# Kernel optimization log

Hardware: AMD Instinct MI355X
Metric: run time of the kernel (lower is better)

## Reference

```python
import math
import jax, jax.numpy as jnp
import numpy as np

B, T, C, H, TOP_K = 2, 2048, 1024, 16, 256
D = C // H  # head_dim = 64


def setup_inputs() -> dict:
    key = jax.random.key(0)
    kx, kq, kk, kv, ko = jax.random.split(key, 5)
    s = 1.0 / math.sqrt(C)
    return {
        "x": jax.random.normal(kx, (B, T, C), dtype=jnp.float32),
        "Wq": jax.random.normal(kq, (C, C), dtype=jnp.float32) * s,
        "Wk": jax.random.normal(kk, (C, C), dtype=jnp.float32) * s,
        "Wv": jax.random.normal(kv, (C, C), dtype=jnp.float32) * s,
        "Wo": jax.random.normal(ko, (C, C), dtype=jnp.float32) * s,
    }


def _sparsify_last_dim_topk(x, keep_k):
    # keep the keep_k largest-|.| entries along the last dim, zero the rest
    a = jnp.abs(x)
    kth = jax.lax.top_k(a, keep_k)[0][..., -1:]  # k-th largest magnitude
    return jnp.where(a >= kth, x, jnp.zeros_like(x))


def reference(x, Wq, Wk, Wv, Wo):
    b, t, c = x.shape
    k_keep = min(TOP_K, t)

    def proj(W):  # nn.Linear (no bias): x @ W.T, then split heads -> [B,H,T,D]
        return (x @ W.T).reshape(b, t, H, D).transpose(0, 2, 1, 3)

    q, k, v = proj(Wq), proj(Wk), proj(Wv)

    # feature-dim sparsification: keep ratio = k_keep / T of head_dim features
    feat_keep = max(1, math.ceil(D * k_keep / t))
    q = _sparsify_last_dim_topk(q, feat_keep)
    k = _sparsify_last_dim_topk(k, feat_keep)
    v = _sparsify_last_dim_topk(v, feat_keep)

    scores = jnp.einsum("bhtd,bhsd->bhts", q, k) / math.sqrt(D)  # [B,H,T,T]
    causal = jnp.tril(jnp.ones((t, t), dtype=bool))  # True = visible
    neg_inf = jnp.float32(-jnp.inf)
    scores = jnp.where(causal, scores, neg_inf)

    # row-wise top-k: keep k_keep largest scores per query row, -inf elsewhere
    kth = jax.lax.top_k(scores, k_keep)[0][..., -1:]
    sparse_scores = jnp.where(scores >= kth, scores, neg_inf)

    attn = jax.nn.softmax(sparse_scores, axis=-1)  # dropout p=0 (eval)
    out = jnp.einsum("bhts,bhsd->bhtd", attn, v)
    out = out.transpose(0, 2, 1, 3).reshape(b, t, c)
    return out @ Wo.T
```

## Files before the change

kernel.cpp:

```cpp
#include <hip/hip_runtime.h>
#include <cstdint>

constexpr int Tn = 2048;
constexpr int Cn = 1024;
constexpr int Mn = 4096;
constexpr int KKEEP = 256;
constexpr int FKEEP = 8;
constexpr unsigned U_NEG_INF = 0x007FFFFFu;

constexpr int NW     = 4;
constexpr int NJMAX  = 32;

__device__ __forceinline__ unsigned umap(float f) {
    unsigned b = __float_as_uint(f);
    return (b & 0x80000000u) ? ~b : (b | 0x80000000u);
}
__device__ __forceinline__ float uunmap(unsigned u) {
    return __uint_as_float((u & 0x80000000u) ? (u ^ 0x80000000u) : ~u);
}

__device__ __forceinline__ unsigned short f2bf(float f) {
    unsigned u = __float_as_uint(f);
    u += 0x7FFFu + ((u >> 16) & 1u);
    return (unsigned short)(u >> 16);
}
struct bfpair { unsigned short h, l; };
__device__ __forceinline__ bfpair split_bf16(float x) {
    bfpair r;
    r.h = f2bf(x);
    r.l = f2bf(x - __uint_as_float((unsigned)r.h << 16));
    return r;
}

__device__ __forceinline__ int   rli(int v, int l)   { return __builtin_amdgcn_readlane(v, l); }
__device__ __forceinline__ float rlf(float v, int l) {
    return __int_as_float(__builtin_amdgcn_readlane(__float_as_int(v), l));
}

typedef __attribute__((ext_vector_type(8))) short          short8v;
typedef __attribute__((ext_vector_type(8))) unsigned short ushort8v;
typedef __attribute__((ext_vector_type(4))) float          f32x4;

__global__ __launch_bounds__(256, 2)
void gemm_nt_3bf16(const float* __restrict__ A,
                   const float* __restrict__ W0, const float* __restrict__ W1,
                   const float* __restrict__ W2,
                   float* __restrict__ O0, float* __restrict__ O1,
                   float* __restrict__ O2)
{
    const float* Wm = (blockIdx.z == 0) ? W0 : (blockIdx.z == 1 ? W1 : W2);
    float*       O  = (blockIdx.z == 0) ? O0 : (blockIdx.z == 1 ? O1 : O2);

    __shared__ unsigned short Ah[128][40], Al[128][40];
    __shared__ unsigned short Bh[128][40], Bl[128][40];

    const int tid  = threadIdx.x;
    const int lane = tid & 63;
    const int wv   = tid >> 6;
    const int wm   = wv >> 1, wn = wv & 1;
    const int fm   = lane & 15;
    const int fq   = lane >> 4;
    const int m0   = blockIdx.y * 128;
    const int n0   = blockIdx.x * 128;

    f32x4 acc[4][4] = {};

    for (int k0 = 0; k0 < Cn; k0 += 32) {
        __syncthreads();
#pragma unroll
        for (int r = 0; r < 2; ++r) {
            const int idx = tid + r * 256;
            const int row = idx >> 2, c8 = (idx & 3) * 8;
            {
                const float* s = &A[(size_t)(m0 + row) * Cn + k0 + c8];
                const float4 x0 = *(const float4*)s, x1 = *(const float4*)(s + 4);
                ushort8v h, l;
                bfpair p;
                p = split_bf16(x0.x); h[0] = p.h; l[0] = p.l;
                p = split_bf16(x0.y); h[1] = p.h; l[1] = p.l;
                p = split_bf16(x0.z); h[2] = p.h; l[2] = p.l;
                p = split_bf16(x0.w); h[3] = p.h; l[3] = p.l;
                p = split_bf16(x1.x); h[4] = p.h; l[4] = p.l;
                p = split_bf16(x1.y); h[5] = p.h; l[5] = p.l;
                p = split_bf16(x1.z); h[6] = p.h; l[6] = p.l;
                p = split_bf16(x1.w); h[7] = p.h; l[7] = p.l;
                *(ushort8v*)&Ah[row][c8] = h;
                *(ushort8v*)&Al[row][c8] = l;
            }
            {
                const float* s = &Wm[(size_t)(n0 + row) * Cn + k0 + c8];
                const float4 x0 = *(const float4*)s, x1 = *(const float4*)(s + 4);
                ushort8v h, l;
                bfpair p;
                p = split_bf16(x0.x); h[0] = p.h; l[0] = p.l;
                p = split_bf16(x0.y); h[1] = p.h; l[1] = p.l;
                p = split_bf16(x0.z); h[2] = p.h; l[2] = p.l;
                p = split_bf16(x0.w); h[3] = p.h; l[3] = p.l;
                p = split_bf16(x1.x); h[4] = p.h; l[4] = p.l;
                p = split_bf16(x1.y); h[5] = p.h; l[5] = p.l;
                p = split_bf16(x1.z); h[6] = p.h; l[6] = p.l;
                p = split_bf16(x1.w); h[7] = p.h; l[7] = p.l;
                *(ushort8v*)&Bh[row][c8] = h;
                *(ushort8v*)&Bl[row][c8] = l;
            }
        }
        __syncthreads();

        short8v ah[4], al[4], bh[4], bl[4];
#pragma unroll
        for (int ti = 0; ti < 4; ++ti) {
            ah[ti] = *(const short8v*)&Ah[wm * 64 + ti * 16 + fm][fq * 8];
            al[ti] = *(const short8v*)&Al[wm * 64 + ti * 16 + fm][fq * 8];
            bh[ti] = *(const short8v*)&Bh[wn * 64 + ti * 16 + fm][fq * 8];
            bl[ti] = *(const short8v*)&Bl[wn * 64 + ti * 16 + fm][fq * 8];
        }
#pragma unroll
        for (int ti = 0; ti < 4; ++ti)
#pragma unroll
            for (int tj = 0; tj < 4; ++tj) {
                acc[ti][tj] = __builtin_amdgcn_mfma_f32_16x16x32_bf16(
                    ah[ti], bh[tj], acc[ti][tj], 0, 0, 0);
                acc[ti][tj] = __builtin_amdgcn_mfma_f32_16x16x32_bf16(
                    ah[ti], bl[tj], acc[ti][tj], 0, 0, 0);
                acc[ti][tj] = __builtin_amdgcn_mfma_f32_16x16x32_bf16(
                    al[ti], bh[tj], acc[ti][tj], 0, 0, 0);
            }
    }

#pragma unroll
    for (int ti = 0; ti < 4; ++ti)
#pragma unroll
        for (int tj = 0; tj < 4; ++tj)
#pragma unroll
            for (int r = 0; r < 4; ++r) {
                const int row = m0 + wm * 64 + ti * 16 + fq * 4 + r;
                const int col = n0 + wn * 64 + tj * 16 + fm;
                O[(size_t)row * Cn + col] = acc[ti][tj][r];
            }
}

__global__ __launch_bounds__(256)
void sparsify_topk(float* __restrict__ Q, float* __restrict__ V)
{
    const int wid  = (blockIdx.x * 256 + threadIdx.x) >> 6;
    const int lane = threadIdx.x & 63;
    const int tensor = wid >> 16;
    const int vec    = wid & 65535;
    float* base = tensor ? V : Q;

    const size_t off = (size_t)vec * 64 + lane;
    const float v = base[off];
    const float a = fabsf(v);

    int cnt = 0;
#pragma unroll
    for (int j = 0; j < 64; ++j) {
        const float aj = __shfl(a, j);
        cnt += (aj > a) ? 1 : 0;
    }
    float cand = (cnt < FKEEP) ? a : 3.402823466e38f;
#pragma unroll
    for (int o = 32; o; o >>= 1) cand = fminf(cand, __shfl_xor(cand, o));
    base[off] = (a >= cand) ? v : 0.0f;
}

__global__ __launch_bounds__(256)
void sparsify_k_t(const float* __restrict__ K, float* __restrict__ KT)
{
    __shared__ float tile[64][65];

    const int tid = threadIdx.x;
    const int w = tid >> 6, lane = tid & 63;
    const int tt = blockIdx.x;
    const int bh = blockIdx.y;
    const int b = bh >> 4, h = bh & 15;
    const int t0 = tt * 64;

#pragma unroll
    for (int k = 0; k < 4; ++k) {
        const int c = tid + k * 256;
        const int row = c >> 4, off = (c & 15) * 4;
        const float4 v4 = *(const float4*)
            &K[(size_t)((b * Tn + t0 + row) * 16 + h) * 64 + off];
        tile[row][off + 0] = v4.x; tile[row][off + 1] = v4.y;
        tile[row][off + 2] = v4.z; tile[row][off + 3] = v4.w;
    }
    __syncthreads();

#pragma unroll 1
    for (int r = w; r < 64; r += 4) {
        const float v = tile[r][lane];
        const float a = fabsf(v);
        int cnt = 0;
#pragma unroll
        for (int j = 0; j < 64; ++j) {
            const float aj = __shfl(a, j);
            cnt += (aj > a) ? 1 : 0;
        }
        float cand = (cnt < FKEEP) ? a : 3.402823466e38f;
#pragma unroll
        for (int o = 32; o; o >>= 1) cand = fminf(cand, __shfl_xor(cand, o));
        tile[r][lane] = (a >= cand) ? v : 0.0f;
    }
    __syncthreads();

#pragma unroll
    for (int k = 0; k < 16; ++k) {
        const int d = w + k * 4;
        KT[(((size_t)bh * 64 + d) << 11) + t0 + lane] = tile[lane][d];
    }
}

__global__ __launch_bounds__(256, 4)
void attn_kernel(const float* __restrict__ Qm, const float* __restrict__ KTm,
                 const float* __restrict__ Vm, float* __restrict__ AO)
{
    __shared__ unsigned hist[NW * 256];
    __shared__ unsigned ctab[NW * 256];
    __shared__ unsigned ptab[NW * 256];

    const int tid  = threadIdx.x;
    const int w    = tid >> 6;
    const int lane = tid & 63;
    const int bh   = blockIdx.y;
    const int b    = bh >> 4;
    const int h    = bh & 15;
    const int t    = blockIdx.x * NW + w;
    const size_t rowoff = ((size_t)(b * Tn + t) << 10) + (h << 6);
    const size_t kvoff  = ((size_t)(b * Tn) << 10) + (h << 6);

    const float q0  = Qm[rowoff + lane];
    const float qsc = q0 * 0.125f;
    const unsigned long long nzm = __ballot(q0 != 0.0f);
    const int nnz = __popcll(nzm);

    const int nj = (t >> 6) + 1;
    const float* ktb = KTm + ((size_t)bh << 17);

    const bool dosel = (t >= KKEEP);
    unsigned* hrow = hist + w * 256;
    hrow[lane] = 0; hrow[64 + lane] = 0; hrow[128 + lane] = 0; hrow[192 + lane] = 0;
    __asm__ volatile("s_waitcnt lgkmcnt(0)" ::: "memory");

    unsigned sv[NJMAX];
    unsigned rowmax = 0u;
    if (nnz == 8) {
        float mq[8]; int moff[8];
        {
            unsigned long long mm = nzm;
#pragma unroll
            for (int i = 0; i < 8; ++i) {
                const int m = (int)__builtin_ctzll(mm); mm &= mm - 1;
                mq[i] = rlf(qsc, m);
                moff[i] = m << 11;
            }
        }
#pragma unroll
        for (int jq = 0; jq < NJMAX / 4; ++jq) {
            const int j0 = jq * 4;
            if (j0 >= nj) {
                sv[j0] = U_NEG_INF; sv[j0 + 1] = U_NEG_INF;
                sv[j0 + 2] = U_NEG_INF; sv[j0 + 3] = U_NEG_INF;
                continue;
            }
            const int c0 = (j0 << 6) + lane;
            if (j0 + 4 <= nj) {
                float s0 = 0.0f, s1 = 0.0f, s2 = 0.0f, s3 = 0.0f;
#pragma unroll
                for (int i = 0; i < 8; ++i) {
                    const float* kpi = ktb + moff[i];
                    s0 += mq[i] * kpi[c0];
                    s1 += mq[i] * kpi[c0 + 64];
                    s2 += mq[i] * kpi[c0 + 128];
                    s3 += mq[i] * kpi[c0 + 192];
                }
                const unsigned v0 = (c0       <= t) ? umap(s0) : U_NEG_INF;
                const unsigned v1 = (c0 +  64 <= t) ? umap(s1) : U_NEG_INF;
                const unsigned v2 = (c0 + 128 <= t) ? umap(s2) : U_NEG_INF;
                const unsigned v3 = (c0 + 192 <= t) ? umap(s3) : U_NEG_INF;
                sv[j0] = v0; sv[j0 + 1] = v1; sv[j0 + 2] = v2; sv[j0 + 3] = v3;
                unsigned m01 = (v0 > v1) ? v0 : v1;
                unsigned m23 = (v2 > v3) ? v2 : v3;
                m01 = (m01 > m23) ? m01 : m23;
                rowmax = (m01 > rowmax) ? m01 : rowmax;
                if (dosel) {
                    atomicAdd(&hrow[v0 >> 24], 1u);
                    atomicAdd(&hrow[v1 >> 24], 1u);
                    atomicAdd(&hrow[v2 >> 24], 1u);
                    atomicAdd(&hrow[v3 >> 24], 1u);
                }
            } else {
#pragma unroll
                for (int k = 0; k < 4; ++k) {
                    const int j = j0 + k;
                    if (j < nj) {
                        const int col = (j << 6) + lane;
                        float s = 0.0f;
#pragma unroll
                        for (int i = 0; i < 8; ++i)
                            s += mq[i] * ktb[moff[i] + col];
                        const unsigned v = (col <= t) ? umap(s) : U_NEG_INF;
                        sv[j] = v;
                        rowmax = (v > rowmax) ? v : rowmax;
                        if (dosel) atomicAdd(&hrow[v >> 24], 1u);
                    } else sv[j] = U_NEG_INF;
                }
            }
        }
    } else {
#pragma unroll
        for (int j = 0; j < NJMAX; ++j) {
            if (j >= nj) { sv[j] = U_NEG_INF; continue; }
            const int col = (j << 6) + lane;
            float s = 0.0f;
            unsigned long long mm = nzm;
            while (mm) {
                const int m = (int)__builtin_ctzll(mm); mm &= mm - 1;
                s += rlf(qsc, m) * ktb[((size_t)m << 11) + col];
            }
            const unsigned val = (col <= t) ? umap(s) : U_NEG_INF;
            sv[j] = val;
            rowmax = (val > rowmax) ? val : rowmax;
            if (dosel) atomicAdd(&hrow[val >> 24], 1u);
        }
    }

#pragma unroll
    for (int o = 32; o; o >>= 1) {
        const unsigned m2 = __shfl_xor(rowmax, o);
        rowmax = (m2 > rowmax) ? m2 : rowmax;
    }
    const float fm = uunmap(rowmax);

    unsigned cur = U_NEG_INF;
    if (dosel) {
        unsigned prefix = 0u, pmask = 0u;
        unsigned r = KKEEP;
#pragma unroll 1
        for (int level = 0; level < 4; ++level) {
            const int sh = 24 - 8 * level;
            if (level) {
                hrow[lane] = 0; hrow[64 + lane] = 0;
                hrow[128 + lane] = 0; hrow[192 + lane] = 0;
                __asm__ volatile("s_waitcnt lgkmcnt(0)" ::: "memory");
#pragma unroll
                for (int j = 0; j < NJMAX; ++j) {
                    if (j < nj) {
                        const int col = (j << 6) + lane;
                        const unsigned v = sv[j];
                        if (col <= t && (v & pmask) == prefix)
                            atomicAdd(&hrow[(v >> sh) & 255u], 1u);
                    }
                }
            }
            __asm__ volatile("s_waitcnt lgkmcnt(0)" ::: "memory");
            const uint4 hv = *(const uint4*)&hrow[lane * 4];
            const unsigned ls = hv.x + hv.y + hv.z + hv.w;
            unsigned sfx = ls;
#pragma unroll
            for (int off = 1; off < 64; off <<= 1) {
                const unsigned tt2 = __shfl_down(sfx, off);
                if (lane + off < 64) sfx += tt2;
            }
            const unsigned excl = sfx - ls;
            const unsigned c3 = excl + hv.w, c2 = c3 + hv.z,
                           c1 = c2 + hv.y,  c0 = c1 + hv.x;
            int bsel = -1; unsigned csel = 0, cnext = 0;
            if      (c3 >= r) { bsel = 4 * lane + 3; csel = c3; cnext = excl; }
            else if (c2 >= r) { bsel = 4 * lane + 2; csel = c2; cnext = c3; }
            else if (c1 >= r) { bsel = 4 * lane + 1; csel = c1; cnext = c2; }
            else if (c0 >= r) { bsel = 4 * lane + 0; csel = c0; cnext = c1; }
            int B = bsel;
#pragma unroll
            for (int off = 32; off; off >>= 1) {
                const int ob = __shfl_xor(B, off);
                B = (ob > B) ? ob : B;
            }
            const unsigned cB  = (unsigned)__shfl((int)csel,  B >> 2);
            const unsigned cB1 = (unsigned)__shfl((int)cnext, B >> 2);
            prefix |= (unsigned)B << sh;
            pmask  |= 255u << sh;
            if (cB == r || level == 3) { cur = prefix; break; }
            r -= cB1;
        }
    }

    unsigned* ct = ctab + w * 256;
    unsigned* cp = ptab + w * 256;
    float ps = 0.0f;
    int cnt = 0; bool ovf = false;
#pragma unroll
    for (int j = 0; j < NJMAX; ++j) {
        if (j >= nj) continue;
        const int col = (j << 6) + lane;
        float pv = 0.0f;
        const unsigned uv = sv[j];
        if (col <= t && uv >= cur) pv = __expf(uunmap(uv) - fm);
        ps += pv;
        const unsigned long long m = __ballot(pv > 0.0f);
        const int c = __popcll(m);
        if (cnt + c <= 256) {
            if (pv > 0.0f) {
                const int pos = cnt + __popcll(m & ((1ull << lane) - 1ull));
                ct[pos] = (unsigned)col;
                cp[pos] = __float_as_uint(pv);
            }
        } else ovf = true;
        cnt += c;
    }
#pragma unroll
    for (int o = 32; o; o >>= 1) ps += __shfl_xor(ps, o);
    const float inv = 1.0f / ps;

    if (!ovf) {
        int   cR[4]; float pR[4];
#pragma unroll
        for (int blk = 0; blk < 4; ++blk) {
            const int idx = blk * 64 + lane;
            cR[blk] = (idx < cnt) ? (int)ct[idx] : 0;
            pR[blk] = (idx < cnt) ? __uint_as_float(cp[idx]) : 0.0f;
        }
        const int g  = lane >> 4;
        const int d0 = (lane & 15) * 4;
        float ax = 0.0f, ay = 0.0f, az = 0.0f, aw = 0.0f;
        const float* __restrict__ vb4 = Vm + kvoff + d0;
        auto do_blk = [&](int blk_c, float blk_p) {
#pragma unroll
            for (int j = 0; j < 16; ++j) {
                const int   c = __shfl(blk_c, 4 * j + g);
                const float p = __shfl(blk_p, 4 * j + g);
                const float4 v4 = *(const float4*)&vb4[(size_t)c * Cn];
                ax += p * v4.x; ay += p * v4.y;
                az += p * v4.z; aw += p * v4.w;
            }
        };
        do_blk(cR[0], pR[0]);
        if (cnt > 64)  do_blk(cR[1], pR[1]);
        if (cnt > 128) do_blk(cR[2], pR[2]);
        if (cnt > 192) do_blk(cR[3], pR[3]);
#pragma unroll
        for (int o = 16; o <= 32; o <<= 1) {
            ax += __shfl_xor(ax, o);
            ay += __shfl_xor(ay, o);
            az += __shfl_xor(az, o);
            aw += __shfl_xor(aw, o);
        }
        if (g == 0) {
            float4 r;
            r.x = ax * inv; r.y = ay * inv; r.z = az * inv; r.w = aw * inv;
            *(float4*)&AO[rowoff + d0] = r;
        }
    } else {
        const float* __restrict__ vcol = Vm + kvoff + lane;
        float acc = 0.0f;
#pragma unroll
        for (int j = 0; j < NJMAX; ++j) {
            if (j >= nj) continue;
            const int col = (j << 6) + lane;
            float pv = 0.0f;
            const unsigned uv = sv[j];
            if (col <= t && uv >= cur) pv = __expf(uunmap(uv) - fm);
            unsigned long long m = __ballot(pv > 0.0f);
            const int cb = j << 6;
            while (m) {
                const int l0 = __builtin_ctzll(m); m &= m - 1;
                const float w0 = __shfl(pv, l0);
                const float v0 = vcol[(size_t)(cb + l0) * Cn];
                float w1 = 0.0f, v1 = 0.0f;
                if (m) {
                    const int l1 = __builtin_ctzll(m); m &= m - 1;
                    w1 = __shfl(pv, l1);
                    v1 = vcol[(size_t)(cb + l1) * Cn];
                }
                acc += w0 * v0;
                acc += w1 * v1;
            }
        }
        AO[rowoff + lane] = acc * inv;
    }
}

extern "C" void kernel_launch(void* const* d_in, const int* in_sizes, int n_in,
                              void* d_out, int out_size, void* d_ws, size_t ws_size,
                              hipStream_t stream)
{
    const float* x  = (const float*)d_in[0];
    const float* Wq = (const float*)d_in[1];
    const float* Wk = (const float*)d_in[2];
    const float* Wv = (const float*)d_in[3];
    const float* Wo = (const float*)d_in[4];
    float* out = (float*)d_out;

    float* Q  = (float*)d_ws;
    float* K  = Q + (size_t)Mn * Cn;
    float* V  = K + (size_t)Mn * Cn;
    float* KT = V + (size_t)Mn * Cn;
    float* AO = K;

    gemm_nt_3bf16<<<dim3(Cn / 128, Mn / 128, 3), 256, 0, stream>>>(
        x, Wq, Wk, Wv, Q, K, V);

    sparsify_topk<<<dim3(2 * 65536 / 4), 256, 0, stream>>>(Q, V);

    sparsify_k_t<<<dim3(32, 32), 256, 0, stream>>>(K, KT);

    attn_kernel<<<dim3(Tn / NW, 32), 256, 0, stream>>>(Q, KT, V, AO);

    gemm_nt_3bf16<<<dim3(Cn / 128, Mn / 128, 1), 256, 0, stream>>>(
        AO, Wo, Wo, Wo, out, out, out);
}
```

Before: 833.9 us.

## Pre-split GEMM operands into bf16 hi/lo once instead of per tile

Adds a presplit kernel that converts x and Wq/Wk/Wv into bf16 hi/lo arrays once, so the QKV GEMM loads ready bf16 tiles instead of re-splitting fp32 on every tile load. The attention kernel now writes its output directly as bf16 hi/lo, so the output projection GEMM only splits Wo. This removes redundant conversion ALU work in the GEMM inner loops. In exchange it adds an extra launch and extra global traffic for the split buffers, and reuses the output and KT scratch memory as staging space.

Result: faster. 798.6 us (-4.2%).

```diff
diff --git a/kernel.cpp b/kernel.cpp
--- a/kernel.cpp
+++ b/kernel.cpp
@@ -41,15 +41,58 @@
 typedef __attribute__((ext_vector_type(8))) unsigned short ushort8v;
 typedef __attribute__((ext_vector_type(4))) float          f32x4;
 
+constexpr size_t XCHUNK = (size_t)Mn * Cn / 8;
+constexpr size_t WCHUNK = (size_t)Cn * Cn / 8;
+constexpr size_t WELEMS = (size_t)Cn * Cn;
+
+__device__ __forceinline__ void split8(const float* s, unsigned short* dh,
+                                       unsigned short* dl, size_t base)
+{
+    const float4 a = *(const float4*)&s[base], b = *(const float4*)&s[base + 4];
+    ushort8v h, l; bfpair p;
+    p = split_bf16(a.x); h[0] = p.h; l[0] = p.l;
+    p = split_bf16(a.y); h[1] = p.h; l[1] = p.l;
+    p = split_bf16(a.z); h[2] = p.h; l[2] = p.l;
+    p = split_bf16(a.w); h[3] = p.h; l[3] = p.l;
+    p = split_bf16(b.x); h[4] = p.h; l[4] = p.l;
+    p = split_bf16(b.y); h[5] = p.h; l[5] = p.l;
+    p = split_bf16(b.z); h[6] = p.h; l[6] = p.l;
+    p = split_bf16(b.w); h[7] = p.h; l[7] = p.l;
+    *(ushort8v*)&dh[base] = h;
+    *(ushort8v*)&dl[base] = l;
+}
+
+__global__ __launch_bounds__(256)
+void presplit(const float* __restrict__ x,  const float* __restrict__ Wq,
+              const float* __restrict__ Wk, const float* __restrict__ Wv,
+              unsigned short* __restrict__ XH, unsigned short* __restrict__ XL,
+              unsigned short* __restrict__ WHL)
+{
+    const size_t cid = (size_t)blockIdx.x * 256 + threadIdx.x;
+    if (cid < XCHUNK) {
+        split8(x, XH, XL, cid * 8);
+    } else {
+        const size_t c2 = cid - XCHUNK;
+        const int    z  = (int)(c2 / WCHUNK);
+        const size_t e  = (c2 % WCHUNK) * 8;
+        const float* src = (z == 0) ? Wq : (z == 1 ? Wk : Wv);
+        unsigned short* dh = WHL + (size_t)z * 2 * WELEMS;
+        unsigned short* dl = dh + WELEMS;
+        split8(src, dh, dl, e);
+    }
+}
+
 __global__ __launch_bounds__(256, 2)
-void gemm_nt_3bf16(const float* __restrict__ A,
-                   const float* __restrict__ W0, const float* __restrict__ W1,
-                   const float* __restrict__ W2,
-                   float* __restrict__ O0, float* __restrict__ O1,
-                   float* __restrict__ O2)
-{
-    const float* Wm = (blockIdx.z == 0) ? W0 : (blockIdx.z == 1 ? W1 : W2);
-    float*       O  = (blockIdx.z == 0) ? O0 : (blockIdx.z == 1 ? O1 : O2);
+void gemm_qkv_ps(const unsigned short* __restrict__ XH,
+                 const unsigned short* __restrict__ XL,
+                 const unsigned short* __restrict__ WHL,
+                 float* __restrict__ O0, float* __restrict__ O1,
+                 float* __restrict__ O2)
+{
+    const int z = blockIdx.z;
+    const unsigned short* WH = WHL + (size_t)z * 2 * WELEMS;
+    const unsigned short* WL = WH + WELEMS;
+    float* O = (z == 0) ? O0 : (z == 1 ? O1 : O2);
 
     __shared__ unsigned short Ah[128][40], Al[128][40];
     __shared__ unsigned short Bh[128][40], Bl[128][40];
@@ -71,24 +114,78 @@
         for (int r = 0; r < 2; ++r) {
             const int idx = tid + r * 256;
             const int row = idx >> 2, c8 = (idx & 3) * 8;
+            const size_t ao = (size_t)(m0 + row) * Cn + k0 + c8;
+            const size_t bo = (size_t)(n0 + row) * Cn + k0 + c8;
+            *(ushort8v*)&Ah[row][c8] = *(const ushort8v*)&XH[ao];
+            *(ushort8v*)&Al[row][c8] = *(const ushort8v*)&XL[ao];
+            *(ushort8v*)&Bh[row][c8] = *(const ushort8v*)&WH[bo];
+            *(ushort8v*)&Bl[row][c8] = *(const ushort8v*)&WL[bo];
+        }
+        __syncthreads();
+
+        short8v ah[4], al[4], bh[4], bl[4];
+#pragma unroll
+        for (int ti = 0; ti < 4; ++ti) {
+            ah[ti] = *(const short8v*)&Ah[wm * 64 + ti * 16 + fm][fq * 8];
+            al[ti] = *(const short8v*)&Al[wm * 64 + ti * 16 + fm][fq * 8];
+            bh[ti] = *(const short8v*)&Bh[wn * 64 + ti * 16 + fm][fq * 8];
+            bl[ti] = *(const short8v*)&Bl[wn * 64 + ti * 16 + fm][fq * 8];
+        }
+#pragma unroll
+        for (int ti = 0; ti < 4; ++ti)
+#pragma unroll
+            for (int tj = 0; tj < 4; ++tj) {
+                acc[ti][tj] = __builtin_amdgcn_mfma_f32_16x16x32_bf16(
+                    ah[ti], bh[tj], acc[ti][tj], 0, 0, 0);
+                acc[ti][tj] = __builtin_amdgcn_mfma_f32_16x16x32_bf16(
+                    ah[ti], bl[tj], acc[ti][tj], 0, 0, 0);
+                acc[ti][tj] = __builtin_amdgcn_mfma_f32_16x16x32_bf16(
+                    al[ti], bh[tj], acc[ti][tj], 0, 0, 0);
+            }
+    }
+
+#pragma unroll
+    for (int ti = 0; ti < 4; ++ti)
+#pragma unroll
+        for (int tj = 0; tj < 4; ++tj)
+#pragma unroll
+            for (int r = 0; r < 4; ++r) {
+                const int row = m0 + wm * 64 + ti * 16 + fq * 4 + r;
+                const int col = n0 + wn * 64 + tj * 16 + fm;
+                O[(size_t)row * Cn + col] = acc[ti][tj][r];
+            }
+}
+
+__global__ __launch_bounds__(256, 2)
+void gemm_out_ps(const unsigned short* __restrict__ AH,
+                 const unsigned short* __restrict__ AL,
+                 const float* __restrict__ Wo, float* __restrict__ O)
+{
+    __shared__ unsigned short Ah[128][40], Al[128][40];
+    __shared__ unsigned short Bh[128][40], Bl[128][40];
+
+    const int tid  = threadIdx.x;
+    const int lane = tid & 63;
+    const int wv   = tid >> 6;
+    const int wm   = wv >> 1, wn = wv & 1;
+    const int fm   = lane & 15;
+    const int fq   = lane >> 4;
+    const int m0   = blockIdx.y * 128;
+    const int n0   = blockIdx.x * 128;
+
+    f32x4 acc[4][4] = {};
+
+    for (int k0 = 0; k0 < Cn; k0 += 32) {
+        __syncthreads();
+#pragma unroll
+        for (int r = 0; r < 2; ++r) {
+            const int idx = tid + r * 256;
+            const int row = idx >> 2, c8 = (idx & 3) * 8;
+            const size_t ao = (size_t)(m0 + row) * Cn + k0 + c8;
+            *(ushort8v*)&Ah[row][c8] = *(const ushort8v*)&AH[ao];
+            *(ushort8v*)&Al[row][c8] = *(const ushort8v*)&AL[ao];
             {
-                const float* s = &A[(size_t)(m0 + row) * Cn + k0 + c8];
-                const float4 x0 = *(const float4*)s, x1 = *(const float4*)(s + 4);
-                ushort8v h, l;
-                bfpair p;
-                p = split_bf16(x0.x); h[0] = p.h; l[0] = p.l;
-                p = split_bf16(x0.y); h[1] = p.h; l[1] = p.l;
-                p = split_bf16(x0.z); h[2] = p.h; l[2] = p.l;
-                p = split_bf16(x0.w); h[3] = p.h; l[3] = p.l;
-                p = split_bf16(x1.x); h[4] = p.h; l[4] = p.l;
-                p = split_bf16(x1.y); h[5] = p.h; l[5] = p.l;
-                p = split_bf16(x1.z); h[6] = p.h; l[6] = p.l;
-                p = split_bf16(x1.w); h[7] = p.h; l[7] = p.l;
-                *(ushort8v*)&Ah[row][c8] = h;
-                *(ushort8v*)&Al[row][c8] = l;
-            }
-            {
-                const float* s = &Wm[(size_t)(n0 + row) * Cn + k0 + c8];
+                const float* s = &Wo[(size_t)(n0 + row) * Cn + k0 + c8];
                 const float4 x0 = *(const float4*)s, x1 = *(const float4*)(s + 4);
                 ushort8v h, l;
                 bfpair p;
@@ -213,7 +310,9 @@
 
 __global__ __launch_bounds__(256, 4)
 void attn_kernel(const float* __restrict__ Qm, const float* __restrict__ KTm,
-                 const float* __restrict__ Vm, float* __restrict__ AO)
+                 const float* __restrict__ Vm,
+                 unsigned short* __restrict__ AOH,
+                 unsigned short* __restrict__ AOL)
 {
     __shared__ unsigned hist[NW * 256];
     __shared__ unsigned ctab[NW * 256];
@@ -446,9 +545,15 @@
             aw += __shfl_xor(aw, o);
         }
         if (g == 0) {
-            float4 r;
-            r.x = ax * inv; r.y = ay * inv; r.z = az * inv; r.w = aw * inv;
-            *(float4*)&AO[rowoff + d0] = r;
+            const float vx = ax * inv, vy = ay * inv,
+                        vz = az * inv, vw = aw * inv;
+            const bfpair px = split_bf16(vx), py = split_bf16(vy),
+                         pz = split_bf16(vz), pw = split_bf16(vw);
+            ushort4 hq, lq;
+            hq.x = px.h; hq.y = py.h; hq.z = pz.h; hq.w = pw.h;
+            lq.x = px.l; lq.y = py.l; lq.z = pz.l; lq.w = pw.l;
+            *(ushort4*)&AOH[rowoff + d0] = hq;
+            *(ushort4*)&AOL[rowoff + d0] = lq;
         }
     } else {
         const float* __restrict__ vcol = Vm + kvoff + lane;
@@ -476,7 +581,10 @@
                 acc += w1 * v1;
             }
         }
-        AO[rowoff + lane] = acc * inv;
+        const float v = acc * inv;
+        const bfpair p = split_bf16(v);
+        AOH[rowoff + lane] = p.h;
+        AOL[rowoff + lane] = p.l;
     }
 }
 
@@ -495,17 +603,25 @@
     float* K  = Q + (size_t)Mn * Cn;
     float* V  = K + (size_t)Mn * Cn;
     float* KT = V + (size_t)Mn * Cn;
-    float* AO = K;
-
-    gemm_nt_3bf16<<<dim3(Cn / 128, Mn / 128, 3), 256, 0, stream>>>(
-        x, Wq, Wk, Wv, Q, K, V);
+
+    unsigned short* XH  = (unsigned short*)d_out;
+    unsigned short* XL  = XH + (size_t)Mn * Cn;
+    unsigned short* WHL = (unsigned short*)KT;
+    unsigned short* AOH = (unsigned short*)K;
+    unsigned short* AOL = AOH + (size_t)Mn * Cn;
+
+    presplit<<<dim3((unsigned)((XCHUNK + 3 * WCHUNK) / 256)), 256, 0, stream>>>(
+        x, Wq, Wk, Wv, XH, XL, WHL);
+
+    gemm_qkv_ps<<<dim3(Cn / 128, Mn / 128, 3), 256, 0, stream>>>(
+        XH, XL, WHL, Q, K, V);
 
     sparsify_topk<<<dim3(2 * 65536 / 4), 256, 0, stream>>>(Q, V);
 
     sparsify_k_t<<<dim3(32, 32), 256, 0, stream>>>(K, KT);
 
-    attn_kernel<<<dim3(Tn / NW, 32), 256, 0, stream>>>(Q, KT, V, AO);
-
-    gemm_nt_3bf16<<<dim3(Cn / 128, Mn / 128, 1), 256, 0, stream>>>(
-        AO, Wo, Wo, Wo, out, out, out);
-}
+    attn_kernel<<<dim3(Tn / NW, 32), 256, 0, stream>>>(Q, KT, V, AOH, AOL);
+
+    gemm_out_ps<<<dim3(Cn / 128, Mn / 128, 1), 256, 0, stream>>>(
+        AOH, AOL, Wo, out);
+}
```
